# Performance work log

Measured on AMD Instinct MI355X. Metric: run time of the kernel, lower is better.

Reference implementation:

```python
import jax, jax.numpy as jnp
import numpy as np
import math

BS, C, NH, NL, NP = 2, 128, 1, 2, 8
SHAPES = np.array([[128, 256], [64, 128]], dtype=np.int64)  # [num_level, (H, W)]
NQ = int(SHAPES[0, 0] * SHAPES[0, 1])  # 32768 queries at level-0 resolution
NV = int((SHAPES[:, 0] * SHAPES[:, 1]).sum())  # 40960


def _offset_bias():
    # replicate init_weights grid bias
    thetas = np.arange(NH, dtype=np.float32) * (2.0 * math.pi / NH)
    grid = np.stack([np.cos(thetas), np.sin(thetas)], -1)
    grid = grid / np.abs(grid).max(-1, keepdims=True)
    grid = np.tile(grid.reshape(NH, 1, 1, 2), (1, NL, NP, 1))
    for i in range(NP):
        grid[:, :, i, :] *= i + 1
    return jnp.asarray(grid.reshape(-1), dtype=jnp.float32)


def setup_inputs() -> dict:
    key = jax.random.key(0)
    ks = jax.random.split(key, 8)
    query = jax.random.normal(ks[0], (BS, NQ, C), dtype=jnp.float32)
    value = jax.random.normal(ks[1], (BS, NV, C), dtype=jnp.float32)
    query_location = jax.random.uniform(ks[2], (BS, NQ, NL, 2), dtype=jnp.float32)
    spatial_shapes = jnp.asarray(SHAPES)
    level_start_index = jnp.asarray(np.concatenate([[0], np.cumsum(SHAPES[:, 0] * SHAPES[:, 1])[:-1]]))
    # params (small random offset weights instead of exact-zero init so offsets depend on query)
    W_off = 0.01 * jax.random.normal(ks[3], (C, NH * NL * NP * 2), dtype=jnp.float32)
    b_off = _offset_bias()
    W_attn = 0.01 * jax.random.normal(ks[4], (C, NH * NL * NP), dtype=jnp.float32)
    b_attn = jnp.zeros((NH * NL * NP,), dtype=jnp.float32)
    lim = 1.0 / np.sqrt(C)
    W_out = jax.random.uniform(ks[5], (C * NH, C), minval=-lim, maxval=lim, dtype=jnp.float32)
    b_out = jnp.zeros((C,), dtype=jnp.float32)
    return {"query": query, "value": value, "query_location": query_location,
            "spatial_shapes": spatial_shapes, "level_start_index": level_start_index,
            "W_off": W_off, "b_off": b_off, "W_attn": W_attn, "b_attn": b_attn,
            "W_out": W_out, "b_out": b_out}


def _ms_deform_attn(value, shapes_np, loc, aw):
    # value: [bs, nv, c]; loc: [bs, nq, nh, nl, np, 2] in [0,1]; aw: [bs, nq, nh, nl, np]
    bs, nq = loc.shape[0], loc.shape[1]
    hd = value.shape[-1] // NH
    out = jnp.zeros((bs, NH, nq, hd), dtype=value.dtype)
    start = 0
    for l in range(NL):
        H, W = int(shapes_np[l, 0]), int(shapes_np[l, 1])
        # [bs, nh, H*W, hd]
        v = value[:, start:start + H * W].reshape(bs, H * W, NH, hd).transpose(0, 2, 1, 3)
        # grid_sample align_corners=False convention: x = gx*W - 0.5 with gx in [0,1]
        x = loc[:, :, :, l, :, 0] * W - 0.5  # [bs, nq, nh, np]
        y = loc[:, :, :, l, :, 1] * H - 0.5
        x0 = jnp.floor(x); y0 = jnp.floor(y)
        lx = (x - x0).transpose(0, 2, 1, 3).reshape(bs, NH, nq * NP)[..., None]
        ly = (y - y0).transpose(0, 2, 1, 3).reshape(bs, NH, nq * NP)[..., None]
        x0i = x0.astype(jnp.int32); y0i = y0.astype(jnp.int32)

        def gat(ix, iy):
            valid = ((ix >= 0) & (ix < W) & (iy >= 0) & (iy < H)).astype(value.dtype)
            idx = jnp.clip(iy, 0, H - 1) * W + jnp.clip(ix, 0, W - 1)
            idx_t = idx.transpose(0, 2, 1, 3).reshape(bs, NH, nq * NP)
            g = jnp.take_along_axis(v, idx_t[..., None], axis=2)  # [bs, nh, nq*np, hd]
            m = valid.transpose(0, 2, 1, 3).reshape(bs, NH, nq * NP)
            return g * m[..., None]

        samp = (gat(x0i, y0i) * (1 - lx) * (1 - ly)
                + gat(x0i + 1, y0i) * lx * (1 - ly)
                + gat(x0i, y0i + 1) * (1 - lx) * ly
                + gat(x0i + 1, y0i + 1) * lx * ly)  # [bs, nh, nq*np, hd]
        w = aw[:, :, :, l].transpose(0, 2, 1, 3).reshape(bs, NH, nq * NP)[..., None]
        out = out + (samp * w).reshape(bs, NH, nq, NP, hd).sum(3)
        start += H * W
    return out.transpose(0, 2, 1, 3).reshape(bs, nq, NH * hd)


def reference(query, value, query_location, spatial_shapes, level_start_index,
              W_off, b_off, W_attn, b_attn, W_out, b_out):
    bs, nq, c = query.shape
    shapes_np = np.asarray(spatial_shapes)
    off = (query @ W_off + b_off).reshape(bs, nq, NH, NL, NP, 2)
    aw = jax.nn.softmax((query @ W_attn + b_attn).reshape(bs, nq, NH, NL * NP), axis=-1)
    aw = aw.reshape(bs, nq, NH, NL, NP)
    # offset_normalizer = [W, H] per level
    norm = jnp.stack([jnp.asarray(shapes_np[:, 1], jnp.float32),
                      jnp.asarray(shapes_np[:, 0], jnp.float32)], -1)  # [nl, 2]
    loc = query_location[:, :, None, :, None, :] + off / norm[None, None, None, :, None, :]
    out = _ms_deform_attn(value, shapes_np, loc, aw)
    return out @ W_out + b_out  # dropout is identity at eval
```

## Files before the change

### kernel.cpp

```cpp
#include <hip/hip_runtime.h>
#include <hip/hip_fp16.h>


#define QB 32

struct __align__(8) h2x2 { __half2 a, b; };

__global__ __launch_bounds__(256) void cvt_value_f16_kernel(
    const float4* __restrict__ in, h2x2* __restrict__ out, int n4)
{
    const int i = blockIdx.x * 256 + threadIdx.x;
    if (i < n4) {
        const float4 f = in[i];
        h2x2 h;
        h.a = __floats2half2_rn(f.x, f.y);
        h.b = __floats2half2_rn(f.z, f.w);
        out[i] = h;
    }
}

#define MSDA_PROLOGUE                                                          \
    float*  q_tile = (float*)smem_u;                                           \
    float4* wo_w   = (float4*)smem_u;                                          \
    int4*   wo_o   = (int4*)(smem_u + QB * 16 * 16);                           \
    const int tid = threadIdx.x;                                               \
    const int r0  = blockIdx.x * QB;                                           \
    {                                                                          \
        const float4* src = (const float4*)query + (size_t)r0 * 32;            \
        float4* dst = (float4*)q_tile;                                         \
        _Pragma("unroll")                                                      \
        for (int i = 0; i < 4; ++i)                                            \
            dst[tid + i * 256] = src[tid + i * 256];                           \
    }                                                                          \
    __syncthreads();                                                           \
    {                                                                          \
        const int jo = tid & 31;                                               \
        const int qb = (tid >> 5) * 4;                                         \
        float s[4] = {0.f, 0.f, 0.f, 0.f};                                     \
        for (int c4 = 0; c4 < 32; ++c4) {                                      \
            const float w0 = Woff[(c4 * 4 + 0) * 32 + jo];                     \
            const float w1 = Woff[(c4 * 4 + 1) * 32 + jo];                     \
            const float w2 = Woff[(c4 * 4 + 2) * 32 + jo];                     \
            const float w3 = Woff[(c4 * 4 + 3) * 32 + jo];                     \
            _Pragma("unroll")                                                  \
            for (int k = 0; k < 4; ++k) {                                      \
                const float4 q4 = *(const float4*)&q_tile[(qb + k) * 128 + c4 * 4]; \
                s[k] += q4.x * w0 + q4.y * w1 + q4.z * w2 + q4.w * w3;         \
            }                                                                  \
        }                                                                      \
        const int l = jo >> 4;                                                 \
        const int d = jo & 1;                                                  \
        const float scale = (d == 0) ? (l == 0 ? 256.f : 128.f)                \
                                     : (l == 0 ? 128.f : 64.f);                \
        const float bo = boff[jo];                                             \
        _Pragma("unroll")                                                      \
        for (int k = 0; k < 4; ++k) {                                          \
            const int row = r0 + qb + k;                                       \
            const float ql = qloc[row * 4 + l * 2 + d];                        \
            coords[(qb + k) * 32 + jo] = ql * scale + (s[k] + bo) - 0.5f;      \
        }                                                                      \
    }                                                                          \
    {                                                                          \
        const int ja = tid & 15;                                               \
        const int qb = (tid >> 4) * 2;                                         \
        float s[2] = {0.f, 0.f};                                               \
        for (int c4 = 0; c4 < 32; ++c4) {                                      \
            const float w0 = Wattn[(c4 * 4 + 0) * 16 + ja];                    \
            const float w1 = Wattn[(c4 * 4 + 1) * 16 + ja];                    \
            const float w2 = Wattn[(c4 * 4 + 2) * 16 + ja];                    \
            const float w3 = Wattn[(c4 * 4 + 3) * 16 + ja];                    \
            _Pragma("unroll")                                                  \
            for (int k = 0; k < 2; ++k) {                                      \
                const float4 q4 = *(const float4*)&q_tile[(qb + k) * 128 + c4 * 4]; \
                s[k] += q4.x * w0 + q4.y * w1 + q4.z * w2 + q4.w * w3;         \
            }                                                                  \
        }                                                                      \
        const float ba = battn[ja];                                            \
        _Pragma("unroll")                                                      \
        for (int k = 0; k < 2; ++k)                                            \
            aws[(qb + k) * 16 + ja] = s[k] + ba;                               \
    }                                                                          \
    __syncthreads();                                                           \
    if (tid < QB) {                                                            \
        float* a = &aws[tid * 16];                                             \
        float m = a[0];                                                        \
        _Pragma("unroll")                                                      \
        for (int j = 1; j < 16; ++j) m = fmaxf(m, a[j]);                       \
        float sum = 0.f;                                                       \
        _Pragma("unroll")                                                      \
        for (int j = 0; j < 16; ++j) {                                         \
            const float e = __expf(a[j] - m);                                  \
            a[j] = e;                                                          \
            sum += e;                                                          \
        }                                                                      \
        const float r = 1.f / sum;                                             \
        _Pragma("unroll")                                                      \
        for (int j = 0; j < 16; ++j) a[j] *= r;                                \
    }                                                                          \
    __syncthreads();                                                           \
    _Pragma("unroll")                                                          \
    for (int e = tid; e < QB * 16; e += 256) {                                 \
        const int q = e >> 4;                                                  \
        const int p = e & 15;                                                  \
        const int l = p >> 3;                                                  \
        const int H = l ? 64 : 128;                                            \
        const int W = l ? 128 : 256;                                           \
        const int S = l ? 32768 : 0;                                           \
        const float x   = coords[q * 32 + p * 2 + 0];                          \
        const float y   = coords[q * 32 + p * 2 + 1];                          \
        const float wgt = aws[q * 16 + p];                                     \
        const float xf = floorf(x), yf = floorf(y);                            \
        const float lx = x - xf, ly = y - yf;                                  \
        const int x0 = (int)xf, y0 = (int)yf;                                  \
        const int x1 = x0 + 1, y1 = y0 + 1;                                    \
        const float hx = 1.f - lx, hy = 1.f - ly;                              \
        float w00 = wgt * hx * hy;                                             \
        float w10 = wgt * lx * hy;                                             \
        float w01 = wgt * hx * ly;                                             \
        float w11 = wgt * lx * ly;                                             \
        if (x0 < 0 || x0 >= W) { w00 = 0.f; w01 = 0.f; }                       \
        if (x1 < 0 || x1 >= W) { w10 = 0.f; w11 = 0.f; }                       \
        if (y0 < 0 || y0 >= H) { w00 = 0.f; w10 = 0.f; }                       \
        if (y1 < 0 || y1 >= H) { w01 = 0.f; w11 = 0.f; }                       \
        const int cx0 = min(max(x0, 0), W - 1);                                \
        const int cx1 = min(max(x1, 0), W - 1);                                \
        const int cy0 = min(max(y0, 0), H - 1);                                \
        const int cy1 = min(max(y1, 0), H - 1);                                \
        wo_w[e] = make_float4(w00, w10, w01, w11);                             \
        wo_o[e] = make_int4((S + cy0 * W + cx0) * 32,                          \
                            (S + cy0 * W + cx1) * 32,                          \
                            (S + cy1 * W + cx0) * 32,                          \
                            (S + cy1 * W + cx1) * 32);                        \
    }                                                                          \
    __syncthreads();

__global__ __launch_bounds__(256, 4) void msda_gather_f16_kernel(
    const float* __restrict__ query,
    const h2x2*  __restrict__ value_h,
    const float* __restrict__ qloc,
    const float* __restrict__ Woff,
    const float* __restrict__ boff,
    const float* __restrict__ Wattn,
    const float* __restrict__ battn,
    float* __restrict__ acc_out)
{
    __shared__ __align__(16) char smem_u[QB * 128 * 4];
    __shared__ float coords[QB * 32];
    __shared__ float aws[QB * 16];
    MSDA_PROLOGUE

    {
        const int wv   = tid >> 6;
        const int lane = tid & 63;
        const int half = lane >> 5;
        const int cl   = lane & 31;
        const h2x2* vb = value_h + (size_t)(blockIdx.x >> 10) * (40960 * 32);
        float4* og = (float4*)acc_out;

        #pragma unroll 1
        for (int i = 0; i < 8; ++i) {
            const int q = wv * 8 + i;
            const int base_e = q * 16;
            float ax = 0.f, ay = 0.f, az = 0.f, aw4 = 0.f;

            int   oa[16], ob[16];
            float wa[16], wb[16];
            #pragma unroll
            for (int p = 0; p < 16; ++p) {
                const float4 w = wo_w[base_e + p];
                const int4   o = wo_o[base_e + p];
                oa[p] = (half ? o.y : o.x) + cl;
                ob[p] = (half ? o.w : o.z) + cl;
                wa[p] = half ? w.y : w.x;
                wb[p] = half ? w.w : w.z;
            }
            h2x2 vA[16], vB[16];
            #pragma unroll
            for (int p = 0; p < 16; ++p) {
                vA[p] = vb[oa[p]];
                vB[p] = vb[ob[p]];
            }
            #pragma unroll
            for (int p = 0; p < 16; ++p) {
                const float2 a0 = __half22float2(vA[p].a);
                const float2 a1 = __half22float2(vA[p].b);
                const float2 b0 = __half22float2(vB[p].a);
                const float2 b1 = __half22float2(vB[p].b);
                ax  += wa[p] * a0.x + wb[p] * b0.x;
                ay  += wa[p] * a0.y + wb[p] * b0.y;
                az  += wa[p] * a1.x + wb[p] * b1.x;
                aw4 += wa[p] * a1.y + wb[p] * b1.y;
            }
            ax  += __shfl_xor(ax, 32, 64);
            ay  += __shfl_xor(ay, 32, 64);
            az  += __shfl_xor(az, 32, 64);
            aw4 += __shfl_xor(aw4, 32, 64);
            if (half == 0)
                og[(size_t)(r0 + q) * 32 + cl] = make_float4(ax, ay, az, aw4);
        }
    }
}

__global__ __launch_bounds__(256, 4) void msda_gather_f32_kernel(
    const float* __restrict__ query,
    const float* __restrict__ value,
    const float* __restrict__ qloc,
    const float* __restrict__ Woff,
    const float* __restrict__ boff,
    const float* __restrict__ Wattn,
    const float* __restrict__ battn,
    float* __restrict__ acc_out)
{
    __shared__ __align__(16) char smem_u[QB * 128 * 4];
    __shared__ float coords[QB * 32];
    __shared__ float aws[QB * 16];
    MSDA_PROLOGUE

    {
        const int wv   = tid >> 6;
        const int lane = tid & 63;
        const int half = lane >> 5;
        const int cl   = lane & 31;
        const float4* vb = (const float4*)value
                         + (size_t)(blockIdx.x >> 10) * (40960 * 32);
        float4* og = (float4*)acc_out;

        #pragma unroll 1
        for (int i = 0; i < 8; ++i) {
            const int q = wv * 8 + i;
            const int base_e = q * 16;
            float ax = 0.f, ay = 0.f, az = 0.f, aw4 = 0.f;

            #pragma unroll 1
            for (int p0 = 0; p0 < 16; p0 += 8) {
                int   oa[8], ob[8];
                float wa[8], wb[8];
                #pragma unroll
                for (int pi = 0; pi < 8; ++pi) {
                    const float4 w = wo_w[base_e + p0 + pi];
                    const int4   o = wo_o[base_e + p0 + pi];
                    oa[pi] = (half ? o.y : o.x) + cl;
                    ob[pi] = (half ? o.w : o.z) + cl;
                    wa[pi] = half ? w.y : w.x;
                    wb[pi] = half ? w.w : w.z;
                }
                float4 vA[8], vB[8];
                #pragma unroll
                for (int pi = 0; pi < 8; ++pi) {
                    vA[pi] = vb[oa[pi]];
                    vB[pi] = vb[ob[pi]];
                }
                #pragma unroll
                for (int pi = 0; pi < 8; ++pi) {
                    ax  += wa[pi] * vA[pi].x + wb[pi] * vB[pi].x;
                    ay  += wa[pi] * vA[pi].y + wb[pi] * vB[pi].y;
                    az  += wa[pi] * vA[pi].z + wb[pi] * vB[pi].z;
                    aw4 += wa[pi] * vA[pi].w + wb[pi] * vB[pi].w;
                }
            }
            ax  += __shfl_xor(ax, 32, 64);
            ay  += __shfl_xor(ay, 32, 64);
            az  += __shfl_xor(az, 32, 64);
            aw4 += __shfl_xor(aw4, 32, 64);
            if (half == 0)
                og[(size_t)(r0 + q) * 32 + cl] = make_float4(ax, ay, az, aw4);
        }
    }
}

#define GR 64

__global__ __launch_bounds__(256, 3) void msda_out_gemm_kernel(
    const float* __restrict__ Wout,
    const float* __restrict__ bout,
    float* __restrict__ out)
{
    __shared__ __align__(16) float a_tile[GR * 68];
    __shared__ __align__(16) float w_tile[64 * 128];
    const int tid  = threadIdx.x;
    const int r0   = blockIdx.x * GR;
    const int trow = tid >> 4;
    const int tcol = tid & 15;

    float4 o[4][2];
    #pragma unroll
    for (int k = 0; k < 4; ++k) {
        o[k][0] = make_float4(0.f, 0.f, 0.f, 0.f);
        o[k][1] = make_float4(0.f, 0.f, 0.f, 0.f);
    }

    #pragma unroll 1
    for (int h = 0; h < 2; ++h) {
        {
            const float4* src = (const float4*)out;
            #pragma unroll
            for (int i = 0; i < 4; ++i) {
                const int t  = tid + i * 256;
                const int r  = t >> 4;
                const int c4 = t & 15;
                const float4 v = src[(size_t)(r0 + r) * 32 + h * 16 + c4];
                *(float4*)&a_tile[r * 68 + c4 * 4] = v;
            }
            const float4* ws = (const float4*)Wout + (size_t)h * 64 * 32;
            float4* wd = (float4*)w_tile;
            #pragma unroll
            for (int i = 0; i < 8; ++i)
                wd[tid + i * 256] = ws[tid + i * 256];
        }
        __syncthreads();

        #pragma unroll 1
        for (int c4 = 0; c4 < 16; ++c4) {
            float4 a4[4];
            #pragma unroll
            for (int k = 0; k < 4; ++k)
                a4[k] = *(const float4*)&a_tile[(trow + 16 * k) * 68 + c4 * 4];
            #pragma unroll
            for (int j = 0; j < 4; ++j) {
                const int ci = c4 * 4 + j;
                const float4 w0 = *(const float4*)&w_tile[ci * 128 + tcol * 8];
                const float4 w1 = *(const float4*)&w_tile[ci * 128 + tcol * 8 + 4];
                #pragma unroll
                for (int k = 0; k < 4; ++k) {
                    const float a = (j == 0) ? a4[k].x : (j == 1) ? a4[k].y
                                  : (j == 2) ? a4[k].z : a4[k].w;
                    o[k][0].x += a * w0.x; o[k][0].y += a * w0.y;
                    o[k][0].z += a * w0.z; o[k][0].w += a * w0.w;
                    o[k][1].x += a * w1.x; o[k][1].y += a * w1.y;
                    o[k][1].z += a * w1.z; o[k][1].w += a * w1.w;
                }
            }
        }
        __syncthreads();
    }

    const float4 b0 = ((const float4*)bout)[tcol * 2];
    const float4 b1 = ((const float4*)bout)[tcol * 2 + 1];
    float4* og = (float4*)out;
    #pragma unroll
    for (int k = 0; k < 4; ++k) {
        const size_t row = (size_t)(r0 + trow + 16 * k);
        float4 v0 = o[k][0], v1 = o[k][1];
        v0.x += b0.x; v0.y += b0.y; v0.z += b0.z; v0.w += b0.w;
        v1.x += b1.x; v1.y += b1.y; v1.z += b1.z; v1.w += b1.w;
        og[row * 32 + tcol * 2]     = v0;
        og[row * 32 + tcol * 2 + 1] = v1;
    }
}

extern "C" void kernel_launch(void* const* d_in, const int* in_sizes, int n_in,
                              void* d_out, int out_size, void* d_ws, size_t ws_size,
                              hipStream_t stream) {
    const float* query = (const float*)d_in[0];
    const float* value = (const float*)d_in[1];
    const float* qloc  = (const float*)d_in[2];
    const float* Woff  = (const float*)d_in[5];
    const float* boff  = (const float*)d_in[6];
    const float* Wattn = (const float*)d_in[7];
    const float* battn = (const float*)d_in[8];
    const float* Wout  = (const float*)d_in[9];
    const float* bout  = (const float*)d_in[10];
    float* out = (float*)d_out;

    const int n_val = 2 * 40960 * 128;
    const size_t f16_bytes = (size_t)n_val * 2;

    if (ws_size >= f16_bytes) {
        h2x2* val16 = (h2x2*)d_ws;
        const int n4 = n_val / 4;
        hipLaunchKernelGGL(cvt_value_f16_kernel, dim3((n4 + 255) / 256), dim3(256),
                           0, stream, (const float4*)value, val16, n4);
        hipLaunchKernelGGL(msda_gather_f16_kernel, dim3(65536 / QB), dim3(256),
                           0, stream,
                           query, (const h2x2*)val16, qloc, Woff, boff, Wattn, battn, out);
    } else {
        hipLaunchKernelGGL(msda_gather_f32_kernel, dim3(65536 / QB), dim3(256),
                           0, stream,
                           query, value, qloc, Woff, boff, Wattn, battn, out);
    }
    hipLaunchKernelGGL(msda_out_gemm_kernel, dim3(65536 / GR), dim3(256), 0, stream,
                       Wout, bout, out);
}
```

Measured before the change: 243.7 us.

## Pack sample table per half-wave, chunk fp16 gather, enlarge output GEMM tile

The sampling table is repacked so each half-wave reads one int4 holding its two weights and two offsets, replacing two selects across a float4 and an int4. The fp16 gather loop is split into two chunks of 8 points to reduce register pressure, and the fp16 convert uses low/high extraction. The output GEMM tile grows from 64 to 128 rows per block, with an interleaved weight-column mapping and fewer blocks per SM. The larger GEMM tile raises register use and lowers occupancy, and its output writes in place could race with other blocks' reads if they overlap.

```diff
diff --git a/kernel.cpp b/kernel.cpp
--- a/kernel.cpp
+++ b/kernel.cpp
@@ -20,9 +20,8 @@
 }
 
 #define MSDA_PROLOGUE                                                          \
-    float*  q_tile = (float*)smem_u;                                           \
-    float4* wo_w   = (float4*)smem_u;                                          \
-    int4*   wo_o   = (int4*)(smem_u + QB * 16 * 16);                           \
+    float* q_tile = (float*)smem_u;                                            \
+    int4*  tab    = (int4*)smem_u;                                             \
     const int tid = threadIdx.x;                                               \
     const int r0  = blockIdx.x * QB;                                           \
     {                                                                          \
@@ -126,11 +125,13 @@
         const int cx1 = min(max(x1, 0), W - 1);                                \
         const int cy0 = min(max(y0, 0), H - 1);                                \
         const int cy1 = min(max(y1, 0), H - 1);                                \
-        wo_w[e] = make_float4(w00, w10, w01, w11);                             \
-        wo_o[e] = make_int4((S + cy0 * W + cx0) * 32,                          \
-                            (S + cy0 * W + cx1) * 32,                          \
-                            (S + cy1 * W + cx0) * 32,                          \
-                            (S + cy1 * W + cx1) * 32);                        \
+        int4 e0, e1;                                                           \
+        e0.x = __float_as_int(w00); e0.y = __float_as_int(w01);                \
+        e0.z = (S + cy0 * W + cx0) * 32; e0.w = (S + cy1 * W + cx0) * 32;      \
+        e1.x = __float_as_int(w10); e1.y = __float_as_int(w11);                \
+        e1.z = (S + cy0 * W + cx1) * 32; e1.w = (S + cy1 * W + cx1) * 32;      \
+        tab[e * 2]     = e0;                                                   \
+        tab[e * 2 + 1] = e1;                                                   \
     }                                                                          \
     __syncthreads();
 
@@ -160,36 +161,37 @@
         #pragma unroll 1
         for (int i = 0; i < 8; ++i) {
             const int q = wv * 8 + i;
-            const int base_e = q * 16;
             float ax = 0.f, ay = 0.f, az = 0.f, aw4 = 0.f;
 
-            int   oa[16], ob[16];
-            float wa[16], wb[16];
-            #pragma unroll
-            for (int p = 0; p < 16; ++p) {
-                const float4 w = wo_w[base_e + p];
-                const int4   o = wo_o[base_e + p];
-                oa[p] = (half ? o.y : o.x) + cl;
-                ob[p] = (half ? o.w : o.z) + cl;
-                wa[p] = half ? w.y : w.x;
-                wb[p] = half ? w.w : w.z;
-            }
-            h2x2 vA[16], vB[16];
-            #pragma unroll
-            for (int p = 0; p < 16; ++p) {
-                vA[p] = vb[oa[p]];
-                vB[p] = vb[ob[p]];
-            }
-            #pragma unroll
-            for (int p = 0; p < 16; ++p) {
-                const float2 a0 = __half22float2(vA[p].a);
-                const float2 a1 = __half22float2(vA[p].b);
-                const float2 b0 = __half22float2(vB[p].a);
-                const float2 b1 = __half22float2(vB[p].b);
-                ax  += wa[p] * a0.x + wb[p] * b0.x;
-                ay  += wa[p] * a0.y + wb[p] * b0.y;
-                az  += wa[p] * a1.x + wb[p] * b1.x;
-                aw4 += wa[p] * a1.y + wb[p] * b1.y;
+            #pragma unroll 1
+            for (int p0 = 0; p0 < 16; p0 += 8) {
+                float wa[8], wb[8];
+                int   oa[8], ob[8];
+                #pragma unroll
+                for (int pi = 0; pi < 8; ++pi) {
+                    const int4 t = tab[((q * 16 + p0 + pi) << 1) + half];
+                    wa[pi] = __int_as_float(t.x);
+                    wb[pi] = __int_as_float(t.y);
+                    oa[pi] = t.z + cl;
+                    ob[pi] = t.w + cl;
+                }
+                h2x2 vA[8], vB[8];
+                #pragma unroll
+                for (int pi = 0; pi < 8; ++pi) {
+                    vA[pi] = vb[oa[pi]];
+                    vB[pi] = vb[ob[pi]];
+                }
+                #pragma unroll
+                for (int pi = 0; pi < 8; ++pi) {
+                    ax  += wa[pi] * __low2float(vA[pi].a);
+                    ay  += wa[pi] * __high2float(vA[pi].a);
+                    az  += wa[pi] * __low2float(vA[pi].b);
+                    aw4 += wa[pi] * __high2float(vA[pi].b);
+                    ax  += wb[pi] * __low2float(vB[pi].a);
+                    ay  += wb[pi] * __high2float(vB[pi].a);
+                    az  += wb[pi] * __low2float(vB[pi].b);
+                    aw4 += wb[pi] * __high2float(vB[pi].b);
+                }
             }
             ax  += __shfl_xor(ax, 32, 64);
             ay  += __shfl_xor(ay, 32, 64);
@@ -228,21 +230,19 @@
         #pragma unroll 1
         for (int i = 0; i < 8; ++i) {
             const int q = wv * 8 + i;
-            const int base_e = q * 16;
             float ax = 0.f, ay = 0.f, az = 0.f, aw4 = 0.f;
 
             #pragma unroll 1
             for (int p0 = 0; p0 < 16; p0 += 8) {
+                float wa[8], wb[8];
                 int   oa[8], ob[8];
-                float wa[8], wb[8];
-                #pragma unroll
-                for (int pi = 0; pi < 8; ++pi) {
-                    const float4 w = wo_w[base_e + p0 + pi];
-                    const int4   o = wo_o[base_e + p0 + pi];
-                    oa[pi] = (half ? o.y : o.x) + cl;
-                    ob[pi] = (half ? o.w : o.z) + cl;
-                    wa[pi] = half ? w.y : w.x;
-                    wb[pi] = half ? w.w : w.z;
+                #pragma unroll
+                for (int pi = 0; pi < 8; ++pi) {
+                    const int4 t = tab[((q * 16 + p0 + pi) << 1) + half];
+                    wa[pi] = __int_as_float(t.x);
+                    wb[pi] = __int_as_float(t.y);
+                    oa[pi] = t.z + cl;
+                    ob[pi] = t.w + cl;
                 }
                 float4 vA[8], vB[8];
                 #pragma unroll
@@ -268,9 +268,9 @@
     }
 }
 
-#define GR 64
-
-__global__ __launch_bounds__(256, 3) void msda_out_gemm_kernel(
+#define GR 128
+
+__global__ __launch_bounds__(256, 2) void msda_out_gemm_kernel(
     const float* __restrict__ Wout,
     const float* __restrict__ bout,
     float* __restrict__ out)
@@ -282,9 +282,9 @@
     const int trow = tid >> 4;
     const int tcol = tid & 15;
 
-    float4 o[4][2];
+    float4 o[8][2];
     #pragma unroll
-    for (int k = 0; k < 4; ++k) {
+    for (int k = 0; k < 8; ++k) {
         o[k][0] = make_float4(0.f, 0.f, 0.f, 0.f);
         o[k][1] = make_float4(0.f, 0.f, 0.f, 0.f);
     }
@@ -294,7 +294,7 @@
         {
             const float4* src = (const float4*)out;
             #pragma unroll
-            for (int i = 0; i < 4; ++i) {
+            for (int i = 0; i < 8; ++i) {
                 const int t  = tid + i * 256;
                 const int r  = t >> 4;
                 const int c4 = t & 15;
@@ -311,17 +311,17 @@
 
         #pragma unroll 1
         for (int c4 = 0; c4 < 16; ++c4) {
-            float4 a4[4];
+            float4 a4[8];
             #pragma unroll
-            for (int k = 0; k < 4; ++k)
+            for (int k = 0; k < 8; ++k)
                 a4[k] = *(const float4*)&a_tile[(trow + 16 * k) * 68 + c4 * 4];
             #pragma unroll
             for (int j = 0; j < 4; ++j) {
                 const int ci = c4 * 4 + j;
-                const float4 w0 = *(const float4*)&w_tile[ci * 128 + tcol * 8];
-                const float4 w1 = *(const float4*)&w_tile[ci * 128 + tcol * 8 + 4];
-                #pragma unroll
-                for (int k = 0; k < 4; ++k) {
+                const float4 w0 = *(const float4*)&w_tile[ci * 128 + tcol * 4];
+                const float4 w1 = *(const float4*)&w_tile[ci * 128 + 64 + tcol * 4];
+                #pragma unroll
+                for (int k = 0; k < 8; ++k) {
                     const float a = (j == 0) ? a4[k].x : (j == 1) ? a4[k].y
                                   : (j == 2) ? a4[k].z : a4[k].w;
                     o[k][0].x += a * w0.x; o[k][0].y += a * w0.y;
@@ -334,17 +334,17 @@
         __syncthreads();
     }
 
-    const float4 b0 = ((const float4*)bout)[tcol * 2];
-    const float4 b1 = ((const float4*)bout)[tcol * 2 + 1];
+    const float4 b0 = ((const float4*)bout)[tcol];
+    const float4 b1 = ((const float4*)bout)[16 + tcol];
     float4* og = (float4*)out;
     #pragma unroll
-    for (int k = 0; k < 4; ++k) {
+    for (int k = 0; k < 8; ++k) {
         const size_t row = (size_t)(r0 + trow + 16 * k);
         float4 v0 = o[k][0], v1 = o[k][1];
         v0.x += b0.x; v0.y += b0.y; v0.z += b0.z; v0.w += b0.w;
         v1.x += b1.x; v1.y += b1.y; v1.z += b1.z; v1.w += b1.w;
-        og[row * 32 + tcol * 2]     = v0;
-        og[row * 32 + tcol * 2 + 1] = v1;
+        og[row * 32 + tcol]      = v0;
+        og[row * 32 + 16 + tcol] = v1;
     }
 }
 
```

Result: faster. 238.4 us (-2.1%).
